# Performance work log

Hardware: AMD Instinct MI355X
Metric: run time of the kernel (lower is better)

The kernel has to match this reference:

```python
import jax, jax.numpy as jnp
import numpy as np

RADIUS = 0.4
NSAMPLE = 32
NORMALIZE_DP = True


def setup_inputs() -> dict:
    key = jax.random.key(0)
    k1, k2, k3 = jax.random.split(key, 3)
    B, N, K, C = 2, 16384, 4096, 128
    xyz = jax.random.normal(k1, (B, N, 3), dtype=jnp.float32)
    new_xyz = jax.random.normal(k2, (B, K, 3), dtype=jnp.float32)
    features = jax.random.normal(k3, (B, C, N), dtype=jnp.float32)
    return {"xyz": xyz, "new_xyz": new_xyz, "features": features}


def _ball_query(radius, nsample, xyz, new_xyz):
    # xyz: (B,N,3), new_xyz: (B,K,3) -> indices (B,K,nsample) int32
    N = xyz.shape[1]
    # squared distances via ||a||^2 + ||b||^2 - 2 a.b  -> (B,K,N)
    d2 = (jnp.sum(new_xyz * new_xyz, -1)[:, :, None]
          + jnp.sum(xyz * xyz, -1)[:, None, :]
          - 2.0 * jnp.einsum('bkd,bnd->bkn', new_xyz, xyz))
    mask = d2 < radius * radius
    # key = point index if inside ball else N (sentinel); take nsample smallest
    key = jnp.where(mask, jnp.arange(N, dtype=jnp.int32), jnp.int32(N))
    neg_top, _ = jax.lax.top_k(-key, nsample)  # (B,K,nsample)
    idx = -neg_top
    # pointnet2 semantics: pad with first in-radius index (0 if ball empty)
    first = idx[..., :1]
    first = jnp.where(first < N, first, 0)
    idx = jnp.where(idx < N, idx, first)
    return idx


def _group(features, idx):
    # features: (B,C,N), idx: (B,K,ns) -> (B,C,K,ns)
    return jax.vmap(lambda f, i: f[:, i])(features, idx)


def reference(xyz, new_xyz, features):
    idx = _ball_query(RADIUS, NSAMPLE, xyz, new_xyz)          # (B,K,ns)
    xyz_t = jnp.transpose(xyz, (0, 2, 1))                      # (B,3,N)
    grouped_xyz = _group(xyz_t, idx)                           # (B,3,K,ns)
    grouped_xyz = grouped_xyz - jnp.transpose(new_xyz, (0, 2, 1))[..., None]
    if NORMALIZE_DP:
        grouped_xyz = grouped_xyz / RADIUS
    grouped_features = _group(features, idx)                   # (B,C,K,ns)
    return (grouped_xyz, grouped_features)
```

## Files before the change

### kernel.cpp

```cpp
#include <hip/hip_runtime.h>

#define BB 2
#define NN 16384
#define KK 4096
#define CC 128
#define SS 32
#define BKK (BB * KK)

typedef float vfloat4 __attribute__((ext_vector_type(4)));

__global__ __launch_bounds__(256) void transpose_prep_kernel(
    const float* __restrict__ feat, const float* __restrict__ xyz,
    float* __restrict__ feat_t, float* __restrict__ xyzw)
{
    __shared__ float tile[64][133];
    const int b  = blockIdx.x >> 8;
    const int n0 = (blockIdx.x & 255) * 64;
    const int t  = threadIdx.x;

    if (t < 64) {
        const int i = b * NN + n0 + t;
        const float* p = xyz + (size_t)i * 3;
        const float x = p[0], y = p[1], z = p[2];
        const float pp = __fadd_rn(__fadd_rn(__fmul_rn(x, x), __fmul_rn(y, y)),
                                   __fmul_rn(z, z));
        vfloat4 v = {x, y, z, pp};
        *(vfloat4*)(xyzw + (size_t)i * 4) = v;
    }

#pragma unroll
    for (int i = 0; i < 8; ++i) {
        const int li = i * 256 + t;
        const int c  = li >> 4;
        const int n4 = (li & 15) * 4;
        const vfloat4 v = *(const vfloat4*)(feat + ((size_t)b * CC + c) * NN + n0 + n4);
        tile[n4 + 0][c] = v.x;
        tile[n4 + 1][c] = v.y;
        tile[n4 + 2][c] = v.z;
        tile[n4 + 3][c] = v.w;
    }
    __syncthreads();

#pragma unroll
    for (int i = 0; i < 8; ++i) {
        const int li = i * 256 + t;
        const int n  = li >> 5;
        const int c4 = (li & 31) * 4;
        vfloat4 v;
        v.x = tile[n][c4 + 0];
        v.y = tile[n][c4 + 1];
        v.z = tile[n][c4 + 2];
        v.w = tile[n][c4 + 3];
        *(vfloat4*)(feat_t + ((size_t)(b * NN + n0 + n)) * CC + c4) = v;
    }
}

__global__ __launch_bounds__(1024) void qsort_kernel(
    const float* __restrict__ new_xyz,
    int* __restrict__ qmap)
{
    __shared__ int hist[128];
    __shared__ int base[128];
    __shared__ unsigned char bk[BKK];

    const int t = threadIdx.x;
    if (t < 128) hist[t] = 0;
    __syncthreads();

#pragma unroll
    for (int c = 0; c < BKK / 1024; ++c) {
        const int q = c * 1024 + t;
        const int b = q >> 12;
        const float* p = new_xyz + (size_t)q * 3;
        const float qq = p[0] * p[0] + p[1] * p[1] + p[2] * p[2];
        int bkt = (int)(qq * 8.0f);
        bkt = bkt > 63 ? 63 : bkt;
        bkt |= (b << 6);
        bk[q] = (unsigned char)bkt;
        atomicAdd(&hist[bkt], 1);
    }
    __syncthreads();

    if (t == 0) {
        int s = 0;
#pragma unroll
        for (int i = 0; i < 128; ++i) { base[i] = s; s += hist[i]; }
    }
    __syncthreads();

#pragma unroll
    for (int c = 0; c < BKK / 1024; ++c) {
        const int q = c * 1024 + t;
        const int pos = atomicAdd(&base[bk[q]], 1);
        qmap[pos] = q;
    }
}

__global__ __launch_bounds__(256) void ball_query_kernel(
    const float* __restrict__ xyzw,
    const float* __restrict__ new_xyz,
    const int* __restrict__ qmap,
    int* __restrict__ idx_buf)
{
    const int wave = threadIdx.x >> 6;
    const int lane = threadIdx.x & 63;
    const int qi   = qmap[blockIdx.x * 4 + wave];
    const int b    = qi >> 12;
    const int k    = qi & (KK - 1);

    const float R2 = (float)(0.4 * 0.4);

    const float* q = new_xyz + (size_t)(b * KK + k) * 3;
    const float qx = q[0], qy = q[1], qz = q[2];
    const float qq = __fadd_rn(__fadd_rn(__fmul_rn(qx, qx), __fmul_rn(qy, qy)),
                               __fmul_rn(qz, qz));

    const vfloat4* xw = (const vfloat4*)xyzw + (size_t)b * NN;
    int* out = idx_buf + (size_t)qi * SS;

    int cnt = 0;
    int first = -1;

    auto process = [&](int base, vfloat4 v) {
        const float dot = __fadd_rn(__fadd_rn(__fmul_rn(qx, v.x), __fmul_rn(qy, v.y)),
                                    __fmul_rn(qz, v.z));
        const float d2 = __fsub_rn(__fadd_rn(qq, v.w), __fmul_rn(2.0f, dot));
        const bool inball = d2 < R2;
        const unsigned long long mask = __ballot(inball);
        if (mask) {
            if (first < 0) first = base + (int)__builtin_ctzll(mask);
            if (inball) {
                const int pos = cnt + __popcll(mask & ((1ull << lane) - 1ull));
                if (pos < SS) out[pos] = base + lane;
            }
            cnt += __popcll(mask);
        }
    };

    vfloat4 v0 = xw[lane];
    vfloat4 v1 = xw[64 + lane];
    vfloat4 v2 = xw[128 + lane];
    vfloat4 v3 = xw[192 + lane];

    for (int base = 0; base < NN; base += 256) {
        const int nb = (base + 256 < NN) ? base + 256 : 0;
        vfloat4 u0 = xw[nb + lane];
        vfloat4 u1 = xw[nb + 64 + lane];
        vfloat4 u2 = xw[nb + 128 + lane];
        vfloat4 u3 = xw[nb + 192 + lane];

        process(base, v0);
        process(base + 64, v1);
        process(base + 128, v2);
        process(base + 192, v3);
        if (cnt >= SS) break;

        v0 = u0; v1 = u1; v2 = u2; v3 = u3;
    }

    const int fill = (first < 0) ? 0 : first;
    if (lane < SS && lane >= cnt) out[lane] = fill;
}

__global__ __launch_bounds__(256) void group_kernel(
    const float* __restrict__ xyzw,
    const float* __restrict__ new_xyz,
    const float* __restrict__ feat_t,
    const int*   __restrict__ idx_buf,
    float* __restrict__ out)
{
    __shared__ float tile[SS * CC];
    __shared__ float txyz[3][SS];

    const int t    = threadIdx.x;
    const int l    = t & 63;
    const int w    = t >> 6;
    const int bk   = blockIdx.x;
    const int b    = bk >> 12;
    const int k    = bk & (KK - 1);
    const int half = l >> 5;
    const int cl   = l & 31;

#pragma unroll
    for (int p = 0; p < 4; ++p) {
        const int r = 8 * w + 2 * p;
        const int s = r + half;
        const int n = idx_buf[bk * SS + s];
        const int chunk = cl ^ ((s >> 2) & 7);
        const float* src = feat_t + ((size_t)(b * NN + n)) * CC + 4 * chunk;
        __builtin_amdgcn_global_load_lds(
            (const __attribute__((address_space(1))) void*)src,
            (__attribute__((address_space(3))) void*)(tile + r * CC),
            16, 0, 0);
    }

    if (t < SS) {
        const int n = idx_buf[bk * SS + t];
        const float* q = new_xyz + (size_t)bk * 3;
        const vfloat4 wv = *((const vfloat4*)xyzw + (size_t)b * NN + n);
        txyz[0][t] = (wv.x - q[0]) / 0.4f;
        txyz[1][t] = (wv.y - q[1]) / 0.4f;
        txyz[2][t] = (wv.z - q[2]) / 0.4f;
    }

    __syncthreads();

    float* out_xyz  = out;
    float* out_feat = out + (size_t)BB * 3 * KK * SS;

    const int sq = t & 7;
    const int c0 = t >> 3;
#pragma unroll
    for (int p = 0; p < 4; ++p) {
        const int c  = c0 + 32 * p;
        const int co = (((c >> 2) ^ sq) << 2) + (c & 3);
        vfloat4 v;
        v.x = tile[(4 * sq + 0) * CC + co];
        v.y = tile[(4 * sq + 1) * CC + co];
        v.z = tile[(4 * sq + 2) * CC + co];
        v.w = tile[(4 * sq + 3) * CC + co];
        __builtin_nontemporal_store(
            v, (vfloat4*)(out_feat + (((size_t)(b * CC + c) * KK + k) * SS + 4 * sq)));
    }

    if (t < 24) {
        const int d   = t >> 3;
        const int sq2 = t & 7;
        const vfloat4 v = *(vfloat4*)&txyz[d][4 * sq2];
        __builtin_nontemporal_store(
            v, (vfloat4*)(out_xyz + (((size_t)(b * 3 + d) * KK + k) * SS + 4 * sq2)));
    }
}

extern "C" void kernel_launch(void* const* d_in, const int* in_sizes, int n_in,
                              void* d_out, int out_size, void* d_ws, size_t ws_size,
                              hipStream_t stream) {
    const float* xyz     = (const float*)d_in[0];
    const float* new_xyz = (const float*)d_in[1];
    const float* feat    = (const float*)d_in[2];
    float* out = (float*)d_out;

    int*   idx_buf = (int*)d_ws;
    float* xyzw    = (float*)((char*)d_ws + (1 << 20));
    float* feat_t  = (float*)((char*)d_ws + (1 << 20) + (512 << 10));
    int*   qmap    = (int*)((char*)d_ws + (1 << 20) + (512 << 10) + (CC * NN * BB) * 4);

    transpose_prep_kernel<<<dim3(BB * (NN / 64)), dim3(256), 0, stream>>>(
        feat, xyz, feat_t, xyzw);

    qsort_kernel<<<dim3(1), dim3(1024), 0, stream>>>(new_xyz, qmap);

    ball_query_kernel<<<dim3(BKK / 4), dim3(256), 0, stream>>>(
        xyzw, new_xyz, qmap, idx_buf);

    group_kernel<<<dim3(BKK), dim3(256), 0, stream>>>(
        xyzw, new_xyz, feat_t, idx_buf, out);
}
```

Before: 92.10 us.

## Merge prep with query sort and co-schedule feature transpose with ball query

The xyz packing and the query bucket sort now share one 33-block launch: block 0 sorts the queries and the other blocks pack xyzw. The feature transpose moves out of the prep kernel and into the ball-query launch as extra blocks with 32-point tiles, so the memory-bound transpose can overlap the compute- and latency-bound ball query. The sort now uses 64 buckets that mix both batches instead of 128 per-batch buckets. This removes one launch and a serial dependency, but every ball-query block now also reserves the transpose's shared-memory tile, which may lower its occupancy.

```diff
diff --git a/kernel.cpp b/kernel.cpp
--- a/kernel.cpp
+++ b/kernel.cpp
@@ -9,17 +9,47 @@
 
 typedef float vfloat4 __attribute__((ext_vector_type(4)));
 
-__global__ __launch_bounds__(256) void transpose_prep_kernel(
-    const float* __restrict__ feat, const float* __restrict__ xyz,
-    float* __restrict__ feat_t, float* __restrict__ xyzw)
+__global__ __launch_bounds__(1024) void prep_sort_kernel(
+    const float* __restrict__ xyz, const float* __restrict__ new_xyz,
+    float* __restrict__ xyzw, int* __restrict__ qmap)
 {
-    __shared__ float tile[64][133];
-    const int b  = blockIdx.x >> 8;
-    const int n0 = (blockIdx.x & 255) * 64;
-    const int t  = threadIdx.x;
-
-    if (t < 64) {
-        const int i = b * NN + n0 + t;
+    const int t = threadIdx.x;
+
+    if (blockIdx.x == 0) {
+        __shared__ int hist[64];
+        __shared__ int base[64];
+        __shared__ unsigned char bk[BKK];
+
+        if (t < 64) hist[t] = 0;
+        __syncthreads();
+
+#pragma unroll
+        for (int c = 0; c < BKK / 1024; ++c) {
+            const int q = c * 1024 + t;
+            const float* p = new_xyz + (size_t)q * 3;
+            const float qq = p[0] * p[0] + p[1] * p[1] + p[2] * p[2];
+            int bkt = (int)(qq * 8.0f);
+            bkt = bkt > 63 ? 63 : bkt;
+            bk[q] = (unsigned char)bkt;
+            atomicAdd(&hist[bkt], 1);
+        }
+        __syncthreads();
+
+        if (t == 0) {
+            int s = 0;
+#pragma unroll
+            for (int i = 0; i < 64; ++i) { base[i] = s; s += hist[i]; }
+        }
+        __syncthreads();
+
+#pragma unroll
+        for (int c = 0; c < BKK / 1024; ++c) {
+            const int q = c * 1024 + t;
+            const int pos = atomicAdd(&base[bk[q]], 1);
+            qmap[pos] = q;
+        }
+    } else {
+        const int i = (blockIdx.x - 1) * 1024 + t;
         const float* p = xyz + (size_t)i * 3;
         const float x = p[0], y = p[1], z = p[2];
         const float pp = __fadd_rn(__fadd_rn(__fmul_rn(x, x), __fmul_rn(y, y)),
@@ -27,139 +57,110 @@
         vfloat4 v = {x, y, z, pp};
         *(vfloat4*)(xyzw + (size_t)i * 4) = v;
     }
-
-#pragma unroll
-    for (int i = 0; i < 8; ++i) {
-        const int li = i * 256 + t;
-        const int c  = li >> 4;
-        const int n4 = (li & 15) * 4;
-        const vfloat4 v = *(const vfloat4*)(feat + ((size_t)b * CC + c) * NN + n0 + n4);
-        tile[n4 + 0][c] = v.x;
-        tile[n4 + 1][c] = v.y;
-        tile[n4 + 2][c] = v.z;
-        tile[n4 + 3][c] = v.w;
-    }
-    __syncthreads();
-
-#pragma unroll
-    for (int i = 0; i < 8; ++i) {
-        const int li = i * 256 + t;
-        const int n  = li >> 5;
-        const int c4 = (li & 31) * 4;
-        vfloat4 v;
-        v.x = tile[n][c4 + 0];
-        v.y = tile[n][c4 + 1];
-        v.z = tile[n][c4 + 2];
-        v.w = tile[n][c4 + 3];
-        *(vfloat4*)(feat_t + ((size_t)(b * NN + n0 + n)) * CC + c4) = v;
-    }
-}
-
-__global__ __launch_bounds__(1024) void qsort_kernel(
-    const float* __restrict__ new_xyz,
-    int* __restrict__ qmap)
-{
-    __shared__ int hist[128];
-    __shared__ int base[128];
-    __shared__ unsigned char bk[BKK];
-
-    const int t = threadIdx.x;
-    if (t < 128) hist[t] = 0;
-    __syncthreads();
-
-#pragma unroll
-    for (int c = 0; c < BKK / 1024; ++c) {
-        const int q = c * 1024 + t;
-        const int b = q >> 12;
-        const float* p = new_xyz + (size_t)q * 3;
-        const float qq = p[0] * p[0] + p[1] * p[1] + p[2] * p[2];
-        int bkt = (int)(qq * 8.0f);
-        bkt = bkt > 63 ? 63 : bkt;
-        bkt |= (b << 6);
-        bk[q] = (unsigned char)bkt;
-        atomicAdd(&hist[bkt], 1);
-    }
-    __syncthreads();
-
-    if (t == 0) {
-        int s = 0;
-#pragma unroll
-        for (int i = 0; i < 128; ++i) { base[i] = s; s += hist[i]; }
-    }
-    __syncthreads();
-
-#pragma unroll
-    for (int c = 0; c < BKK / 1024; ++c) {
-        const int q = c * 1024 + t;
-        const int pos = atomicAdd(&base[bk[q]], 1);
-        qmap[pos] = q;
-    }
-}
-
-__global__ __launch_bounds__(256) void ball_query_kernel(
+}
+
+__global__ __launch_bounds__(256) void ball_transpose_kernel(
     const float* __restrict__ xyzw,
     const float* __restrict__ new_xyz,
     const int* __restrict__ qmap,
-    int* __restrict__ idx_buf)
+    const float* __restrict__ feat,
+    int* __restrict__ idx_buf,
+    float* __restrict__ feat_t)
 {
-    const int wave = threadIdx.x >> 6;
-    const int lane = threadIdx.x & 63;
-    const int qi   = qmap[blockIdx.x * 4 + wave];
-    const int b    = qi >> 12;
-    const int k    = qi & (KK - 1);
-
-    const float R2 = (float)(0.4 * 0.4);
-
-    const float* q = new_xyz + (size_t)(b * KK + k) * 3;
-    const float qx = q[0], qy = q[1], qz = q[2];
-    const float qq = __fadd_rn(__fadd_rn(__fmul_rn(qx, qx), __fmul_rn(qy, qy)),
-                               __fmul_rn(qz, qz));
-
-    const vfloat4* xw = (const vfloat4*)xyzw + (size_t)b * NN;
-    int* out = idx_buf + (size_t)qi * SS;
-
-    int cnt = 0;
-    int first = -1;
-
-    auto process = [&](int base, vfloat4 v) {
-        const float dot = __fadd_rn(__fadd_rn(__fmul_rn(qx, v.x), __fmul_rn(qy, v.y)),
-                                    __fmul_rn(qz, v.z));
-        const float d2 = __fsub_rn(__fadd_rn(qq, v.w), __fmul_rn(2.0f, dot));
-        const bool inball = d2 < R2;
-        const unsigned long long mask = __ballot(inball);
-        if (mask) {
-            if (first < 0) first = base + (int)__builtin_ctzll(mask);
-            if (inball) {
-                const int pos = cnt + __popcll(mask & ((1ull << lane) - 1ull));
-                if (pos < SS) out[pos] = base + lane;
+    __shared__ float tile[32][133];
+
+    const int t = threadIdx.x;
+
+    if (blockIdx.x < BKK / 4) {
+        const int wave = t >> 6;
+        const int lane = t & 63;
+        const int qi   = qmap[blockIdx.x * 4 + wave];
+        const int b    = qi >> 12;
+        const int k    = qi & (KK - 1);
+
+        const float R2 = (float)(0.4 * 0.4);
+
+        const float* q = new_xyz + (size_t)(b * KK + k) * 3;
+        const float qx = q[0], qy = q[1], qz = q[2];
+        const float qq = __fadd_rn(__fadd_rn(__fmul_rn(qx, qx), __fmul_rn(qy, qy)),
+                                   __fmul_rn(qz, qz));
+
+        const vfloat4* xw = (const vfloat4*)xyzw + (size_t)b * NN;
+        int* out = idx_buf + (size_t)qi * SS;
+
+        int cnt = 0;
+        int first = -1;
+
+        auto process = [&](int base, vfloat4 v) {
+            const float dot = __fadd_rn(__fadd_rn(__fmul_rn(qx, v.x), __fmul_rn(qy, v.y)),
+                                        __fmul_rn(qz, v.z));
+            const float d2 = __fsub_rn(__fadd_rn(qq, v.w), __fmul_rn(2.0f, dot));
+            const bool inball = d2 < R2;
+            const unsigned long long mask = __ballot(inball);
+            if (mask) {
+                if (first < 0) first = base + (int)__builtin_ctzll(mask);
+                if (inball) {
+                    const int pos = cnt + __popcll(mask & ((1ull << lane) - 1ull));
+                    if (pos < SS) out[pos] = base + lane;
+                }
+                cnt += __popcll(mask);
             }
-            cnt += __popcll(mask);
-        }
-    };
-
-    vfloat4 v0 = xw[lane];
-    vfloat4 v1 = xw[64 + lane];
-    vfloat4 v2 = xw[128 + lane];
-    vfloat4 v3 = xw[192 + lane];
-
-    for (int base = 0; base < NN; base += 256) {
-        const int nb = (base + 256 < NN) ? base + 256 : 0;
-        vfloat4 u0 = xw[nb + lane];
-        vfloat4 u1 = xw[nb + 64 + lane];
-        vfloat4 u2 = xw[nb + 128 + lane];
-        vfloat4 u3 = xw[nb + 192 + lane];
-
-        process(base, v0);
-        process(base + 64, v1);
-        process(base + 128, v2);
-        process(base + 192, v3);
-        if (cnt >= SS) break;
-
-        v0 = u0; v1 = u1; v2 = u2; v3 = u3;
-    }
-
-    const int fill = (first < 0) ? 0 : first;
-    if (lane < SS && lane >= cnt) out[lane] = fill;
+        };
+
+        vfloat4 v0 = xw[lane];
+        vfloat4 v1 = xw[64 + lane];
+        vfloat4 v2 = xw[128 + lane];
+        vfloat4 v3 = xw[192 + lane];
+
+        for (int base = 0; base < NN; base += 256) {
+            const int nb = (base + 256 < NN) ? base + 256 : 0;
+            vfloat4 u0 = xw[nb + lane];
+            vfloat4 u1 = xw[nb + 64 + lane];
+            vfloat4 u2 = xw[nb + 128 + lane];
+            vfloat4 u3 = xw[nb + 192 + lane];
+
+            process(base, v0);
+            process(base + 64, v1);
+            process(base + 128, v2);
+            process(base + 192, v3);
+            if (cnt >= SS) break;
+
+            v0 = u0; v1 = u1; v2 = u2; v3 = u3;
+        }
+
+        const int fill = (first < 0) ? 0 : first;
+        if (lane < SS && lane >= cnt) out[lane] = fill;
+    } else {
+        const int tb = blockIdx.x - BKK / 4;
+        const int b  = tb >> 9;
+        const int n0 = (tb & 511) * 32;
+
+#pragma unroll
+        for (int i = 0; i < 4; ++i) {
+            const int li = i * 256 + t;
+            const int c  = li >> 3;
+            const int n4 = (li & 7) * 4;
+            const vfloat4 v = *(const vfloat4*)(feat + ((size_t)b * CC + c) * NN + n0 + n4);
+            tile[n4 + 0][c] = v.x;
+            tile[n4 + 1][c] = v.y;
+            tile[n4 + 2][c] = v.z;
+            tile[n4 + 3][c] = v.w;
+        }
+        __syncthreads();
+
+#pragma unroll
+        for (int i = 0; i < 4; ++i) {
+            const int li = i * 256 + t;
+            const int n  = li >> 5;
+            const int c4 = (li & 31) * 4;
+            vfloat4 v;
+            v.x = tile[n][c4 + 0];
+            v.y = tile[n][c4 + 1];
+            v.z = tile[n][c4 + 2];
+            v.w = tile[n][c4 + 3];
+            *(vfloat4*)(feat_t + ((size_t)(b * NN + n0 + n)) * CC + c4) = v;
+        }
+    }
 }
 
 __global__ __launch_bounds__(256) void group_kernel(
@@ -245,13 +246,11 @@
     float* feat_t  = (float*)((char*)d_ws + (1 << 20) + (512 << 10));
     int*   qmap    = (int*)((char*)d_ws + (1 << 20) + (512 << 10) + (CC * NN * BB) * 4);
 
-    transpose_prep_kernel<<<dim3(BB * (NN / 64)), dim3(256), 0, stream>>>(
-        feat, xyz, feat_t, xyzw);
-
-    qsort_kernel<<<dim3(1), dim3(1024), 0, stream>>>(new_xyz, qmap);
-
-    ball_query_kernel<<<dim3(BKK / 4), dim3(256), 0, stream>>>(
-        xyzw, new_xyz, qmap, idx_buf);
+    prep_sort_kernel<<<dim3(33), dim3(1024), 0, stream>>>(
+        xyz, new_xyz, xyzw, qmap);
+
+    ball_transpose_kernel<<<dim3(BKK / 4 + BB * (NN / 32)), dim3(256), 0, stream>>>(
+        xyzw, new_xyz, qmap, feat, idx_buf, feat_t);
 
     group_kernel<<<dim3(BKK), dim3(256), 0, stream>>>(
         xyzw, new_xyz, feat_t, idx_buf, out);
```

Measured after the change: 82.67 us. -10.2%, faster.
